# Performance work log

Measured on AMD Instinct MI355X. Metric: run time of the kernel, lower is better.

The kernel has to match this reference:

```python
import jax, jax.numpy as jnp
import numpy as np

TEMPERATURE = 0.07
HARD_NEG_RATIO = 0.5
B, D, N_CLASSES = 2048, 512, 100


def setup_inputs() -> dict:
    key = jax.random.key(0)
    kf, kl = jax.random.split(key)
    features = jax.random.normal(kf, (B, D), dtype=jnp.float32)
    # L2-normalize as is standard for SupCon embeddings (keeps logits well-scaled)
    features = features / jnp.linalg.norm(features, axis=1, keepdims=True)
    labels = jax.random.randint(kl, (B,), 0, N_CLASSES, dtype=jnp.int64)
    return {"features": features, "labels": labels}


def reference(features, labels):
    b = features.shape[0]
    dt = features.dtype
    lab = labels.reshape(-1, 1)
    mask = (lab == lab.T).astype(dt)                       # [B,B] positives (incl. self)
    adc = (features @ features.T) / TEMPERATURE            # [B,B] logits
    logits_max = jax.lax.stop_gradient(jnp.max(adc, axis=1, keepdims=True))
    logits = adc - logits_max                              # row-stabilized
    logits_mask = 1.0 - jnp.eye(b, dtype=dt)               # exclude self
    negative_mask = (1.0 - mask) * logits_mask
    neg_b = negative_mask > 0

    # top-k hard-negative threshold: k-th largest negative logit (global over all pairs).
    # k is data-dependent, so use a full descending sort + dynamic gather (jit-safe).
    flat = jnp.where(neg_b, logits, -jnp.inf).ravel()      # [B*B]
    sorted_desc = -jnp.sort(-flat)
    n_neg = jnp.sum(neg_b)
    k = jnp.maximum(1, (HARD_NEG_RATIO * n_neg).astype(jnp.int32))  # floor, >=1
    threshold = sorted_desc[k - 1]
    hard_negatives_mask = ((logits >= threshold) & neg_b).astype(dt)

    final_mask = jnp.minimum(mask + hard_negatives_mask, 1.0) * logits_mask
    row_pos = final_mask.sum(axis=1)
    single_samples = (row_pos == 0).astype(dt)

    exp_logits = jnp.exp(logits) * logits_mask
    log_prob = logits - jnp.log(exp_logits.sum(axis=1, keepdims=True) + 1e-12)
    mean_log_prob_pos = (final_mask * log_prob).sum(axis=1) / (row_pos + single_samples)
    loss_vec = -mean_log_prob_pos * (1.0 - single_samples)
    loss = loss_vec.sum() / (b - single_samples.sum())
    return (loss, hard_negatives_mask, final_mask)
```

## Files before the change

### kernel.cpp

```cpp
#include <hip/hip_runtime.h>
#include <cstddef>

constexpr int Bn   = 2048;
constexpr int Dn   = 512;
constexpr int NCLS = 100;
constexpr unsigned WWIN = 32768;
constexpr int NH = 32768;


struct Ctl {
  unsigned above;
  unsigned candCount;
  unsigned singles;
  unsigned done;
  float    thrF;
  unsigned pad1;
  double   lossSum;
  unsigned hist[NH];
  unsigned done8[128];
  unsigned sing8[128];
};
static_assert(offsetof(Ctl, hist) == 32, "zero loop covers head + hist + slices");

__device__ inline unsigned key_of(float L) {
  unsigned u = __float_as_uint(L);
  return (u & 0x80000000u) ? ~u : (u | 0x80000000u);
}
__device__ inline float key_to_float(unsigned key) {
  unsigned u = (key & 0x80000000u) ? (key ^ 0x80000000u) : ~key;
  return __uint_as_float(u);
}
__device__ inline unsigned wlo_key() {
  const float c0 = -1.0f / 0.07f;
  return key_of(c0) - (WWIN / 2);
}
__device__ inline void store16_a4(float* p, float4 v) {
  __builtin_memcpy((void*)p, &v, 16);
}
__device__ inline void agent_store_f64(double* p, double v) {
  __hip_atomic_store(p, v, __ATOMIC_RELAXED, __HIP_MEMORY_SCOPE_AGENT);
}
__device__ inline void agent_store_u32(unsigned* p, unsigned v) {
  __hip_atomic_store(p, v, __ATOMIC_RELAXED, __HIP_MEMORY_SCOPE_AGENT);
}

__global__ __launch_bounds__(64) void rowdot_k(const float* __restrict__ F,
                                               float* __restrict__ rm, Ctl* c) {
  const int i = blockIdx.x * 64 + threadIdx.x;
  const float4* p = (const float4*)(F + (size_t)i * Dn);
  float acc = 0.0f;
#pragma unroll 16
  for (int q = 0; q < 128; ++q) {
    const float4 f = p[q];
    acc = __builtin_fmaf(f.x, f.x, acc);
    acc = __builtin_fmaf(f.y, f.y, acc);
    acc = __builtin_fmaf(f.z, f.z, acc);
    acc = __builtin_fmaf(f.w, f.w, acc);
  }
  rm[i] = acc / 0.07f;
  unsigned* cz = (unsigned*)c;
  for (int idx = i; idx < 8 + NH + 256; idx += 2048) cz[idx] = 0;
}

__global__ __launch_bounds__(256) void gemm_adc(const float* __restrict__ F,
                                                const float* __restrict__ rm,
                                                const int* __restrict__ labels,
                                                float* __restrict__ adc, Ctl* c) {
  __shared__ float smem[8704];
  __shared__ int slabi[64], slabj[64];
  __shared__ float rmiA[64], rmjA[64];
  __shared__ unsigned abcnt;
  __shared__ unsigned amlast;
  const int t = threadIdx.x;
  int r = 0;
  { const int idx = blockIdx.x; while ((r + 1) * (r + 2) / 2 <= idx) ++r; }
  const int cc = blockIdx.x - r * (r + 1) / 2;
  const int i0 = r * 64, j0 = cc * 64;

  const int tx = t & 15, ty = t >> 4;
  const int lrow = t >> 2, lq = t & 3;

  if (t < 64) {
    slabi[t] = labels[i0 + t]; rmiA[t] = rm[i0 + t];
    slabj[t] = labels[j0 + t]; rmjA[t] = rm[j0 + t];
  }
  if (t == 0) abcnt = 0;

  float acc[4][4] = {};
  const float* Ab = F + (size_t)(i0 + lrow) * Dn;
  const float* Bb = F + (size_t)(j0 + lrow) * Dn;
  float* As = smem;
  float* Bs = smem + 4352;

  float4 a0 = *(const float4*)(Ab + lq * 4);
  float4 a1 = *(const float4*)(Ab + lq * 4 + 16);
  float4 b0 = *(const float4*)(Bb + lq * 4);
  float4 b1 = *(const float4*)(Bb + lq * 4 + 16);
  {
    const int k0 = lq * 4;
    As[(k0 + 0) * 68 + lrow] = a0.x; As[(k0 + 1) * 68 + lrow] = a0.y;
    As[(k0 + 2) * 68 + lrow] = a0.z; As[(k0 + 3) * 68 + lrow] = a0.w;
    As[(k0 + 16) * 68 + lrow] = a1.x; As[(k0 + 17) * 68 + lrow] = a1.y;
    As[(k0 + 18) * 68 + lrow] = a1.z; As[(k0 + 19) * 68 + lrow] = a1.w;
    Bs[(k0 + 0) * 68 + lrow] = b0.x; Bs[(k0 + 1) * 68 + lrow] = b0.y;
    Bs[(k0 + 2) * 68 + lrow] = b0.z; Bs[(k0 + 3) * 68 + lrow] = b0.w;
    Bs[(k0 + 16) * 68 + lrow] = b1.x; Bs[(k0 + 17) * 68 + lrow] = b1.y;
    Bs[(k0 + 18) * 68 + lrow] = b1.z; Bs[(k0 + 19) * 68 + lrow] = b1.w;
  }
  __syncthreads();

  for (int ch = 0; ch < 16; ++ch) {
    const int cur = ch & 1, nxt = cur ^ 1;
    if (ch < 15) {
      const int kg = (ch + 1) * 32;
      a0 = *(const float4*)(Ab + kg + lq * 4);
      a1 = *(const float4*)(Ab + kg + lq * 4 + 16);
      b0 = *(const float4*)(Bb + kg + lq * 4);
      b1 = *(const float4*)(Bb + kg + lq * 4 + 16);
    }
    const float* Ac = As + cur * 2176;
    const float* Bc = Bs + cur * 2176;
#pragma unroll
    for (int k = 0; k < 32; ++k) {
      const float4 av = *(const float4*)(Ac + k * 68 + ty * 4);
      const float4 bv = *(const float4*)(Bc + k * 68 + tx * 4);
      const float aa[4] = {av.x, av.y, av.z, av.w};
      const float bb[4] = {bv.x, bv.y, bv.z, bv.w};
#pragma unroll
      for (int m = 0; m < 4; ++m)
#pragma unroll
        for (int n = 0; n < 4; ++n)
          acc[m][n] = __builtin_fmaf(aa[m], bb[n], acc[m][n]);
    }
    if (ch < 15) {
      const int k0 = lq * 4;
      float* An = As + nxt * 2176;
      float* Bm = Bs + nxt * 2176;
      An[(k0 + 0) * 68 + lrow] = a0.x; An[(k0 + 1) * 68 + lrow] = a0.y;
      An[(k0 + 2) * 68 + lrow] = a0.z; An[(k0 + 3) * 68 + lrow] = a0.w;
      An[(k0 + 16) * 68 + lrow] = a1.x; An[(k0 + 17) * 68 + lrow] = a1.y;
      An[(k0 + 18) * 68 + lrow] = a1.z; An[(k0 + 19) * 68 + lrow] = a1.w;
      Bm[(k0 + 0) * 68 + lrow] = b0.x; Bm[(k0 + 1) * 68 + lrow] = b0.y;
      Bm[(k0 + 2) * 68 + lrow] = b0.z; Bm[(k0 + 3) * 68 + lrow] = b0.w;
      Bm[(k0 + 16) * 68 + lrow] = b1.x; Bm[(k0 + 17) * 68 + lrow] = b1.y;
      Bm[(k0 + 18) * 68 + lrow] = b1.z; Bm[(k0 + 19) * 68 + lrow] = b1.w;
    }
    __syncthreads();
  }

  float v[4][4];
#pragma unroll
  for (int m = 0; m < 4; ++m) {
#pragma unroll
    for (int n = 0; n < 4; ++n) v[m][n] = acc[m][n] / 0.07f;
    float4 q = {v[m][0], v[m][1], v[m][2], v[m][3]};
    *(float4*)&adc[(size_t)(i0 + ty * 4 + m) * Bn + j0 + tx * 4] = q;
  }
  if (r != cc) {
    __syncthreads();
    float* T = smem;
#pragma unroll
    for (int m = 0; m < 4; ++m)
#pragma unroll
      for (int n = 0; n < 4; ++n)
        T[(tx * 4 + n) * 68 + (ty * 4 + m)] = v[m][n];
    __syncthreads();
#pragma unroll
    for (int e = 0; e < 4; ++e) {
      const int row2 = e * 16 + ty;
      *(float4*)&adc[(size_t)(j0 + row2) * Bn + i0 + tx * 4] =
          *(const float4*)(T + row2 * 68 + tx * 4);
    }
  }

  __syncthreads();
  const unsigned klo = wlo_key(), khi = klo + WWIN;
  unsigned myab = 0;
#pragma unroll
  for (int m = 0; m < 4; ++m) {
    const int gi = i0 + ty * 4 + m;
    const int li = slabi[ty * 4 + m];
    const float rmi = rmiA[ty * 4 + m];
#pragma unroll
    for (int n = 0; n < 4; ++n) {
      const int gj = j0 + tx * 4 + n;
      if (gi == gj || li == slabj[tx * 4 + n]) continue;
      const unsigned key = key_of(v[m][n] - rmi);
      if (key >= khi) ++myab;
      else if (key >= klo) atomicAdd(&c->hist[key - klo], 1u);
      if (r != cc) {
        const unsigned key2 = key_of(v[m][n] - rmjA[tx * 4 + n]);
        if (key2 >= khi) ++myab;
        else if (key2 >= klo) atomicAdd(&c->hist[key2 - klo], 1u);
      }
    }
  }
  if (myab) atomicAdd(&abcnt, myab);
  __syncthreads();
  if (t == 0 && abcnt) atomicAdd(&c->above, abcnt);

  __syncthreads();
  if (t == 0) {
    const int sl = (int)(blockIdx.x & 7);
    unsigned am = 0u;
    if (atomicAdd(&c->done8[sl * 16], 1u) == 65u)
      am = (atomicAdd(&c->done, 1u) == 7u) ? 1u : 0u;
    amlast = am;
  }
  __syncthreads();
  if (!amlast) return;

  unsigned* s_cnt  = (unsigned*)smem;
  unsigned* s_tsum = (unsigned*)smem + 128;
  unsigned* s_scan = (unsigned*)smem + 384;
  if (t < 128) s_cnt[t] = 0;
  __syncthreads();
  for (int j = t; j < Bn; j += 256) atomicAdd(&s_cnt[labels[j]], 1u);
  __syncthreads();
  s_scan[t] = (t < NCLS) ? s_cnt[t] * s_cnt[t] : 0u;
  __syncthreads();
#pragma unroll
  for (int off = 128; off > 0; off >>= 1) {
    if (t < off) s_scan[t] += s_scan[t + off];
    __syncthreads();
  }
  unsigned kk = (((unsigned)Bn * Bn) - s_scan[0]) >> 1;
  if (kk < 1u) kk = 1u;
  __syncthreads();

  const uint4* hp = (const uint4*)c->hist;
  unsigned s = 0;
#pragma unroll 8
  for (int bq = 0; bq < 32; ++bq) {
    const uint4 vq = hp[t * 32 + bq];
    s += vq.x + vq.y + vq.z + vq.w;
  }
  s_tsum[t] = s;
  s_scan[t] = s;
  __syncthreads();
#pragma unroll
  for (int off = 1; off < 256; off <<= 1) {
    const unsigned add = (t + off < 256) ? s_scan[t + off] : 0u;
    __syncthreads();
    s_scan[t] += add;
    __syncthreads();
  }
  const unsigned above = c->above;
  unsigned cum = above + s_scan[t] - s_tsum[t];
  int fbin = -1;
#pragma unroll 8
  for (int bq = 31; bq >= 0; --bq) {
    const uint4 vq = hp[t * 32 + bq];
    const unsigned hq[4] = {vq.x, vq.y, vq.z, vq.w};
#pragma unroll
    for (int u = 3; u >= 0; --u) {
      if (cum < kk && cum + hq[u] >= kk) fbin = t * 128 + bq * 4 + u;
      cum += hq[u];
    }
  }
  if (fbin >= 0) c->thrF = key_to_float(klo + (unsigned)fbin);
}

__global__ __launch_bounds__(256) void final_k(const float* __restrict__ adc,
                                               const int* __restrict__ labels,
                                               Ctl* c,
                                               float* __restrict__ out,
                                               double* __restrict__ lsum_g,
                                               unsigned* __restrict__ scnt_g) {
  __shared__ int slab[Bn];
  __shared__ double lsum[8];
  __shared__ unsigned sflag[8];
  __shared__ unsigned amlast;
  const int t = threadIdx.x;
  const int lane = t & 63, w = t >> 6;
#pragma unroll
  for (int e = 0; e < 2; ++e)
    ((int4*)slab)[t + 256 * e] = ((const int4*)labels)[t + 256 * e];
  __syncthreads();
  const float thr = c->thrF;
  float* __restrict__ ohnm = out + 1;
  float* __restrict__ ofin = out + 1 + (size_t)Bn * Bn;

#pragma unroll
  for (int rr = 0; rr < 2; ++rr) {
    const int i = blockIdx.x * 8 + rr * 4 + w;
    const int li = slab[i];
    const float rm = adc[(size_t)i * Bn + i];
    const float4* rowp = (const float4*)(adc + (size_t)i * Bn);
    float se = 0.0f, sp = 0.0f;
    int pc = 0;
#pragma unroll
    for (int q = 0; q < 8; ++q) {
      const int j4 = lane + 64 * q;
      const float4 vv = rowp[j4];
      const int jb = j4 * 4;
      const float vs[4] = {vv.x, vv.y, vv.z, vv.w};
      float qh[4], qf[4];
#pragma unroll
      for (int u = 0; u < 4; ++u) {
        const int j = jb + u;
        const float L = vs[u] - rm;
        const bool offd = (j != i);
        const bool same = (slab[j] == li);
        const bool hnm  = offd && !same && (L >= thr);
        const bool fin  = offd && (same || hnm);
        if (offd) se += __expf(L);
        if (fin)  { sp += L; ++pc; }
        qh[u] = hnm ? 1.0f : 0.0f;
        qf[u] = fin ? 1.0f : 0.0f;
      }
      float4 h4 = {qh[0], qh[1], qh[2], qh[3]};
      float4 f4 = {qf[0], qf[1], qf[2], qf[3]};
      store16_a4(&ohnm[(size_t)i * Bn + jb], h4);
      store16_a4(&ofin[(size_t)i * Bn + jb], f4);
    }
    float pcf = (float)pc;
#pragma unroll
    for (int o = 32; o > 0; o >>= 1) {
      se  += __shfl_down(se,  o, 64);
      sp  += __shfl_down(sp,  o, 64);
      pcf += __shfl_down(pcf, o, 64);
    }
    if (lane == 0) {
      const double P = (double)pcf;
      const bool single = (P == 0.0);
      const double mlpp = ((double)sp - P * log((double)se + 1e-12)) / (P + (single ? 1.0 : 0.0));
      lsum[w * 2 + rr]  = single ? 0.0 : -mlpp;
      sflag[w * 2 + rr] = single ? 1u : 0u;
    }
  }
  __syncthreads();
  if (t == 0) {
    double ls = 0.0;
    unsigned sc = 0;
#pragma unroll
    for (int e = 0; e < 8; ++e) { ls += lsum[e]; sc += sflag[e]; }
    agent_store_f64(&lsum_g[blockIdx.x], ls);
    agent_store_u32(&scnt_g[blockIdx.x], sc);
    asm volatile("s_waitcnt vmcnt(0)" ::: "memory");
    const int sl = (int)(blockIdx.x & 7);
    unsigned am = 0u;
    if (atomicAdd(&c->sing8[sl * 16], 1u) == 31u)
      am = (atomicAdd(&c->singles, 1u) == 7u) ? 1u : 0u;
    amlast = am;
  }
  __syncthreads();
  if (!amlast) return;

  double ls = lsum_g[t];
  unsigned sc = scnt_g[t];
#pragma unroll
  for (int o = 32; o > 0; o >>= 1) {
    ls += __shfl_down(ls, o, 64);
    sc += __shfl_down(sc, o, 64);
  }
  if (lane == 0) { lsum[w] = ls; sflag[w] = sc; }
  __syncthreads();
  if (t == 0) {
    const double tot = lsum[0] + lsum[1] + lsum[2] + lsum[3];
    const unsigned sg = sflag[0] + sflag[1] + sflag[2] + sflag[3];
    out[0] = (float)(tot / ((double)Bn - (double)sg));
  }
}

extern "C" void kernel_launch(void* const* d_in, const int* in_sizes, int n_in,
                              void* d_out, int out_size, void* d_ws, size_t ws_size,
                              hipStream_t stream) {
  const float* F      = (const float*)d_in[0];
  const int*   labels = (const int*)d_in[1];
  float* out = (float*)d_out;

  char* ws = (char*)d_ws;
  Ctl*      c      = (Ctl*)ws;
  float*    rm     = (float*)(ws + 786432);
  double*   lsum_g = (double*)(ws + 802816);
  unsigned* scnt_g = (unsigned*)(ws + 806912);
  float*    adc    = (float*)(ws + (1u << 20));

  rowdot_k<<<32, 64, 0, stream>>>(F, rm, c);
  gemm_adc<<<528, 256, 0, stream>>>(F, rm, labels, adc, c);
  final_k<<<256, 256, 0, stream>>>(adc, labels, c, out, lsum_g, scnt_g);
}
```

Before: 149.0 us.

## Split each symmetric GEMM tile into two 64x32 half-tiles across blocks

The symmetric-tile GEMM kernel now launches twice as many blocks of 128 threads, each computing a 64x32 half of a 64x64 lower-triangle tile. Global-to-shared loads, the transposed mirror write and the last-block histogram scan are reworked for the new thread count, and the completion counter threshold is updated. The aim is more blocks in flight across the GPU's compute units. In exchange each block loads its A strip twice and has less reuse per block.

```diff
diff --git a/kernel.cpp b/kernel.cpp
--- a/kernel.cpp
+++ b/kernel.cpp
@@ -62,50 +62,50 @@
   for (int idx = i; idx < 8 + NH + 256; idx += 2048) cz[idx] = 0;
 }
 
-__global__ __launch_bounds__(256) void gemm_adc(const float* __restrict__ F,
+__global__ __launch_bounds__(128) void gemm_adc(const float* __restrict__ F,
                                                 const float* __restrict__ rm,
                                                 const int* __restrict__ labels,
                                                 float* __restrict__ adc, Ctl* c) {
-  __shared__ float smem[8704];
-  __shared__ int slabi[64], slabj[64];
-  __shared__ float rmiA[64], rmjA[64];
+  __shared__ float smem[6656];
+  __shared__ int slabi[64], slabj[32];
+  __shared__ float rmiA[64], rmjA[32];
   __shared__ unsigned abcnt;
   __shared__ unsigned amlast;
   const int t = threadIdx.x;
+  const int tile = (int)(blockIdx.x >> 1), h = (int)(blockIdx.x & 1);
   int r = 0;
-  { const int idx = blockIdx.x; while ((r + 1) * (r + 2) / 2 <= idx) ++r; }
-  const int cc = blockIdx.x - r * (r + 1) / 2;
-  const int i0 = r * 64, j0 = cc * 64;
-
-  const int tx = t & 15, ty = t >> 4;
-  const int lrow = t >> 2, lq = t & 3;
-
-  if (t < 64) {
-    slabi[t] = labels[i0 + t]; rmiA[t] = rm[i0 + t];
-    slabj[t] = labels[j0 + t]; rmjA[t] = rm[j0 + t];
-  }
+  { while ((r + 1) * (r + 2) / 2 <= tile) ++r; }
+  const int cc = tile - r * (r + 1) / 2;
+  const int i0 = r * 64, j0 = cc * 64 + h * 32;
+
+  const int tx = t & 7, ty = t >> 3;
+  const int lrowA = t >> 1, lkhA = (t & 1) * 16;
+  const int lrowB = t >> 2, lkqB = (t & 3) * 8;
+
+  if (t < 64) { slabi[t] = labels[i0 + t]; rmiA[t] = rm[i0 + t]; }
+  if (t < 32) { slabj[t] = labels[j0 + t]; rmjA[t] = rm[j0 + t]; }
   if (t == 0) abcnt = 0;
 
   float acc[4][4] = {};
-  const float* Ab = F + (size_t)(i0 + lrow) * Dn;
-  const float* Bb = F + (size_t)(j0 + lrow) * Dn;
+  const float* Ab = F + (size_t)(i0 + lrowA) * Dn + lkhA;
+  const float* Bb = F + (size_t)(j0 + lrowB) * Dn + lkqB;
   float* As = smem;
   float* Bs = smem + 4352;
 
-  float4 a0 = *(const float4*)(Ab + lq * 4);
-  float4 a1 = *(const float4*)(Ab + lq * 4 + 16);
-  float4 b0 = *(const float4*)(Bb + lq * 4);
-  float4 b1 = *(const float4*)(Bb + lq * 4 + 16);
+  float4 a0 = *(const float4*)(Ab);
+  float4 a1 = *(const float4*)(Ab + 4);
+  float4 a2 = *(const float4*)(Ab + 8);
+  float4 a3 = *(const float4*)(Ab + 12);
+  float4 b0 = *(const float4*)(Bb);
+  float4 b1 = *(const float4*)(Bb + 4);
   {
-    const int k0 = lq * 4;
-    As[(k0 + 0) * 68 + lrow] = a0.x; As[(k0 + 1) * 68 + lrow] = a0.y;
-    As[(k0 + 2) * 68 + lrow] = a0.z; As[(k0 + 3) * 68 + lrow] = a0.w;
-    As[(k0 + 16) * 68 + lrow] = a1.x; As[(k0 + 17) * 68 + lrow] = a1.y;
-    As[(k0 + 18) * 68 + lrow] = a1.z; As[(k0 + 19) * 68 + lrow] = a1.w;
-    Bs[(k0 + 0) * 68 + lrow] = b0.x; Bs[(k0 + 1) * 68 + lrow] = b0.y;
-    Bs[(k0 + 2) * 68 + lrow] = b0.z; Bs[(k0 + 3) * 68 + lrow] = b0.w;
-    Bs[(k0 + 16) * 68 + lrow] = b1.x; Bs[(k0 + 17) * 68 + lrow] = b1.y;
-    Bs[(k0 + 18) * 68 + lrow] = b1.z; Bs[(k0 + 19) * 68 + lrow] = b1.w;
+    const float av[16] = {a0.x, a0.y, a0.z, a0.w, a1.x, a1.y, a1.z, a1.w,
+                          a2.x, a2.y, a2.z, a2.w, a3.x, a3.y, a3.z, a3.w};
+    const float bv[8]  = {b0.x, b0.y, b0.z, b0.w, b1.x, b1.y, b1.z, b1.w};
+#pragma unroll
+    for (int q = 0; q < 16; ++q) As[(lkhA + q) * 68 + lrowA] = av[q];
+#pragma unroll
+    for (int q = 0; q < 8; ++q)  Bs[(lkqB + q) * 36 + lrowB] = bv[q];
   }
   __syncthreads();
 
@@ -113,19 +113,21 @@
     const int cur = ch & 1, nxt = cur ^ 1;
     if (ch < 15) {
       const int kg = (ch + 1) * 32;
-      a0 = *(const float4*)(Ab + kg + lq * 4);
-      a1 = *(const float4*)(Ab + kg + lq * 4 + 16);
-      b0 = *(const float4*)(Bb + kg + lq * 4);
-      b1 = *(const float4*)(Bb + kg + lq * 4 + 16);
+      a0 = *(const float4*)(Ab + kg);
+      a1 = *(const float4*)(Ab + kg + 4);
+      a2 = *(const float4*)(Ab + kg + 8);
+      a3 = *(const float4*)(Ab + kg + 12);
+      b0 = *(const float4*)(Bb + kg);
+      b1 = *(const float4*)(Bb + kg + 4);
     }
     const float* Ac = As + cur * 2176;
-    const float* Bc = Bs + cur * 2176;
+    const float* Bc = Bs + cur * 1152;
 #pragma unroll
     for (int k = 0; k < 32; ++k) {
-      const float4 av = *(const float4*)(Ac + k * 68 + ty * 4);
-      const float4 bv = *(const float4*)(Bc + k * 68 + tx * 4);
-      const float aa[4] = {av.x, av.y, av.z, av.w};
-      const float bb[4] = {bv.x, bv.y, bv.z, bv.w};
+      const float4 av4 = *(const float4*)(Ac + k * 68 + ty * 4);
+      const float4 bv4 = *(const float4*)(Bc + k * 36 + tx * 4);
+      const float aa[4] = {av4.x, av4.y, av4.z, av4.w};
+      const float bb[4] = {bv4.x, bv4.y, bv4.z, bv4.w};
 #pragma unroll
       for (int m = 0; m < 4; ++m)
 #pragma unroll
@@ -133,17 +135,15 @@
           acc[m][n] = __builtin_fmaf(aa[m], bb[n], acc[m][n]);
     }
     if (ch < 15) {
-      const int k0 = lq * 4;
+      const float av[16] = {a0.x, a0.y, a0.z, a0.w, a1.x, a1.y, a1.z, a1.w,
+                            a2.x, a2.y, a2.z, a2.w, a3.x, a3.y, a3.z, a3.w};
+      const float bv[8]  = {b0.x, b0.y, b0.z, b0.w, b1.x, b1.y, b1.z, b1.w};
       float* An = As + nxt * 2176;
-      float* Bm = Bs + nxt * 2176;
-      An[(k0 + 0) * 68 + lrow] = a0.x; An[(k0 + 1) * 68 + lrow] = a0.y;
-      An[(k0 + 2) * 68 + lrow] = a0.z; An[(k0 + 3) * 68 + lrow] = a0.w;
-      An[(k0 + 16) * 68 + lrow] = a1.x; An[(k0 + 17) * 68 + lrow] = a1.y;
-      An[(k0 + 18) * 68 + lrow] = a1.z; An[(k0 + 19) * 68 + lrow] = a1.w;
-      Bm[(k0 + 0) * 68 + lrow] = b0.x; Bm[(k0 + 1) * 68 + lrow] = b0.y;
-      Bm[(k0 + 2) * 68 + lrow] = b0.z; Bm[(k0 + 3) * 68 + lrow] = b0.w;
-      Bm[(k0 + 16) * 68 + lrow] = b1.x; Bm[(k0 + 17) * 68 + lrow] = b1.y;
-      Bm[(k0 + 18) * 68 + lrow] = b1.z; Bm[(k0 + 19) * 68 + lrow] = b1.w;
+      float* Bm = Bs + nxt * 1152;
+#pragma unroll
+      for (int q = 0; q < 16; ++q) An[(lkhA + q) * 68 + lrowA] = av[q];
+#pragma unroll
+      for (int q = 0; q < 8; ++q)  Bm[(lkqB + q) * 36 + lrowB] = bv[q];
     }
     __syncthreads();
   }
@@ -165,12 +165,11 @@
       for (int n = 0; n < 4; ++n)
         T[(tx * 4 + n) * 68 + (ty * 4 + m)] = v[m][n];
     __syncthreads();
-#pragma unroll
-    for (int e = 0; e < 4; ++e) {
-      const int row2 = e * 16 + ty;
-      *(float4*)&adc[(size_t)(j0 + row2) * Bn + i0 + tx * 4] =
-          *(const float4*)(T + row2 * 68 + tx * 4);
-    }
+    const int row2 = t >> 2, seg = (t & 3) * 16;
+#pragma unroll
+    for (int e = 0; e < 4; ++e)
+      *(float4*)&adc[(size_t)(j0 + row2) * Bn + i0 + seg + e * 4] =
+          *(const float4*)(T + row2 * 68 + seg + e * 4);
   }
 
   __syncthreads();
@@ -203,7 +202,7 @@
   if (t == 0) {
     const int sl = (int)(blockIdx.x & 7);
     unsigned am = 0u;
-    if (atomicAdd(&c->done8[sl * 16], 1u) == 65u)
+    if (atomicAdd(&c->done8[sl * 16], 1u) == 131u)
       am = (atomicAdd(&c->done, 1u) == 7u) ? 1u : 0u;
     amlast = am;
   }
@@ -212,15 +211,15 @@
 
   unsigned* s_cnt  = (unsigned*)smem;
   unsigned* s_tsum = (unsigned*)smem + 128;
-  unsigned* s_scan = (unsigned*)smem + 384;
-  if (t < 128) s_cnt[t] = 0;
-  __syncthreads();
-  for (int j = t; j < Bn; j += 256) atomicAdd(&s_cnt[labels[j]], 1u);
+  unsigned* s_scan = (unsigned*)smem + 256;
+  s_cnt[t] = 0;
+  __syncthreads();
+  for (int j = t; j < Bn; j += 128) atomicAdd(&s_cnt[labels[j]], 1u);
   __syncthreads();
   s_scan[t] = (t < NCLS) ? s_cnt[t] * s_cnt[t] : 0u;
   __syncthreads();
 #pragma unroll
-  for (int off = 128; off > 0; off >>= 1) {
+  for (int off = 64; off > 0; off >>= 1) {
     if (t < off) s_scan[t] += s_scan[t + off];
     __syncthreads();
   }
@@ -231,16 +230,16 @@
   const uint4* hp = (const uint4*)c->hist;
   unsigned s = 0;
 #pragma unroll 8
-  for (int bq = 0; bq < 32; ++bq) {
-    const uint4 vq = hp[t * 32 + bq];
+  for (int bq = 0; bq < 64; ++bq) {
+    const uint4 vq = hp[t * 64 + bq];
     s += vq.x + vq.y + vq.z + vq.w;
   }
   s_tsum[t] = s;
   s_scan[t] = s;
   __syncthreads();
 #pragma unroll
-  for (int off = 1; off < 256; off <<= 1) {
-    const unsigned add = (t + off < 256) ? s_scan[t + off] : 0u;
+  for (int off = 1; off < 128; off <<= 1) {
+    const unsigned add = (t + off < 128) ? s_scan[t + off] : 0u;
     __syncthreads();
     s_scan[t] += add;
     __syncthreads();
@@ -249,12 +248,12 @@
   unsigned cum = above + s_scan[t] - s_tsum[t];
   int fbin = -1;
 #pragma unroll 8
-  for (int bq = 31; bq >= 0; --bq) {
-    const uint4 vq = hp[t * 32 + bq];
+  for (int bq = 63; bq >= 0; --bq) {
+    const uint4 vq = hp[t * 64 + bq];
     const unsigned hq[4] = {vq.x, vq.y, vq.z, vq.w};
 #pragma unroll
     for (int u = 3; u >= 0; --u) {
-      if (cum < kk && cum + hq[u] >= kk) fbin = t * 128 + bq * 4 + u;
+      if (cum < kk && cum + hq[u] >= kk) fbin = t * 256 + bq * 4 + u;
       cum += hq[u];
     }
   }
@@ -378,6 +377,6 @@
   float*    adc    = (float*)(ws + (1u << 20));
 
   rowdot_k<<<32, 64, 0, stream>>>(F, rm, c);
-  gemm_adc<<<528, 256, 0, stream>>>(F, rm, labels, adc, c);
+  gemm_adc<<<1056, 128, 0, stream>>>(F, rm, labels, adc, c);
   final_k<<<256, 256, 0, stream>>>(adc, labels, c, out, lsum_g, scnt_g);
 }
```

After: 154.3 us. 3.6% more time.
